# Kernel tuning notes

Hardware: AMD Instinct MI355X
Metric: run time of the kernel (lower is better)

Reference implementation:

```python
import jax, jax.numpy as jnp
import numpy as np

N, C, H, K = 4096, 512, 128, 3
NEG = -jnp.inf


def _linear(x, W, b):
    return x @ W.T + b


def _lrelu(x):
    return jnp.where(x > 0, x, 0.01 * x)  # nn.LeakyReLU default slope


def _cos_sim(x, y):
    # torch cal_cos_similarity: xy / (|x| |y|^T), NaN (0/0) -> 0
    xy = x @ y.T
    den = jnp.linalg.norm(x, axis=1, keepdims=True) * jnp.linalg.norm(y, axis=1, keepdims=True).T
    return xy / jnp.where(den == 0, 1.0, den)


def setup_inputs() -> dict:
    key = jax.random.key(0)
    ks = jax.random.split(key, 24)
    x_hidden = jax.random.normal(ks[0], (N, H), jnp.float32)
    cm = (jax.random.uniform(ks[1], (N, C)) < 0.05).astype(jnp.float32)
    # ensure every concept has at least one member stock (no empty concepts)
    cm = cm.at[jnp.arange(C) % N, jnp.arange(C)].set(1.0)
    market_value = jax.random.uniform(ks[2], (N,), jnp.float32, 0.1, 1.0)
    s = 1.0 / np.sqrt(H)
    inp = {"x_hidden": x_hidden, "concept_matrix": cm, "market_value": market_value}
    names = ["ps", "ps_fore", "ps_back", "hs", "hs_fore", "hs_back", "indi"]
    for i, n in enumerate(names):
        inp[f"W_{n}"] = jax.random.uniform(ks[3 + 2 * i], (H, H), jnp.float32, -s, s)
        inp[f"b_{n}"] = jax.random.uniform(ks[4 + 2 * i], (H,), jnp.float32, -s, s)
    inp["W_out"] = jax.random.uniform(ks[20], (1, H), jnp.float32, -s, s)
    inp["b_out"] = jax.random.uniform(ks[21], (1,), jnp.float32, -s, s)
    return inp


def reference(x_hidden, concept_matrix, market_value,
              W_ps, b_ps, W_ps_fore, b_ps_fore, W_ps_back, b_ps_back,
              W_hs, b_hs, W_hs_fore, b_hs_fore, W_hs_back, b_hs_back,
              W_indi, b_indi, W_out, b_out):
    x = x_hidden
    n = x.shape[0]
    # --- predefined-concept (ps) branch ---
    s2c = concept_matrix * market_value[:, None]                     # [N,C]
    s2c_den = s2c.sum(0)[None, :] * concept_matrix + 1.0
    s2c = s2c / s2c_den
    hidden = s2c.T @ x                                               # [C,H]
    valid1 = hidden.sum(1) != 0                                      # row-filter mask
    s2c2 = jax.nn.softmax(x @ hidden.T, axis=0)                      # softmax over stocks
    hidden = (s2c2.T @ x) * valid1[:, None]                          # [C,H]
    c2s = jax.nn.softmax(jnp.where(valid1[None, :], _cos_sim(x, hidden), NEG), axis=1)
    p_shared = _linear(c2s @ hidden, W_ps, b_ps)
    p_back = _linear(p_shared, W_ps_back, b_ps_back)
    out_ps = _lrelu(_linear(p_shared, W_ps_fore, b_ps_fore))
    # --- hidden-concept (hs) branch ---
    h = x - p_back
    hs2c = _cos_sim(h, h)                                            # [N,N]
    diag = jnp.diagonal(hs2c)
    hs2c = hs2c * (1.0 - jnp.eye(n, dtype=h.dtype))
    idx = jax.lax.top_k(hs2c, K)[1]                                  # [N,K]
    mask = jnp.zeros((n, n), h.dtype).at[jnp.arange(n)[:, None], idx].set(1.0)
    hs2c = hs2c * mask
    hs2c = hs2c + jnp.diag((hs2c.sum(0) != 0).astype(h.dtype) * diag)
    hidden2 = hs2c.T @ h                                             # [N,H]
    valid2 = hidden2.sum(1) != 0
    hidden2 = hidden2 * valid2[:, None]
    hc2s = jax.nn.softmax(jnp.where(valid2[None, :], _cos_sim(h, hidden2), NEG), axis=1)
    h_shared = _linear(hc2s @ hidden2, W_hs, b_hs)
    h_back = _linear(h_shared, W_hs_back, b_hs_back)
    out_hs = _lrelu(_linear(h_shared, W_hs_fore, b_hs_fore))
    # --- individual branch ---
    indiv = x - p_back - h_back
    out_indi = _lrelu(_linear(indiv, W_indi, b_indi))
    all_info = out_ps + out_hs + out_indi
    return _linear(all_info, W_out, b_out).squeeze()                 # [N]
```

## Files before the change

kernel.cpp:

```cpp
#include <hip/hip_runtime.h>
#include <hip/hip_fp16.h>
#include <math.h>

#define N 4096
#define C 512
#define H 128
#define PAD 40

typedef __attribute__((ext_vector_type(8))) short bf16x8;
typedef __attribute__((ext_vector_type(4))) float f32x4;


__device__ inline float wave_reduce_sum(float v) {
#pragma unroll
  for (int m = 32; m; m >>= 1) v += __shfl_xor(v, m);
  return v;
}

__device__ inline float lrelu(float v) { return v > 0.f ? v : 0.01f * v; }

__device__ inline bool better(float v, int j, float w, int k) {
  return (v > w) || (v == w && j < k);
}

__device__ inline void top3_ins(float v, int j, float& v0, int& j0,
                                float& v1, int& j1, float& v2, int& j2) {
  if (better(v, j, v0, j0)) { v2 = v1; j2 = j1; v1 = v0; j1 = j0; v0 = v; j0 = j; }
  else if (better(v, j, v1, j1)) { v2 = v1; j2 = j1; v1 = v; j1 = j; }
  else if (better(v, j, v2, j2)) { v2 = v; j2 = j; }
}

__device__ inline void ins5(float s, int j, float v[5], int jx[5]) {
  if (!better(s, j, v[4], jx[4])) return;
  if (better(s, j, v[0], jx[0])) {
    v[4]=v[3]; jx[4]=jx[3]; v[3]=v[2]; jx[3]=jx[2]; v[2]=v[1]; jx[2]=jx[1];
    v[1]=v[0]; jx[1]=jx[0]; v[0]=s; jx[0]=j;
  } else if (better(s, j, v[1], jx[1])) {
    v[4]=v[3]; jx[4]=jx[3]; v[3]=v[2]; jx[3]=jx[2]; v[2]=v[1]; jx[2]=jx[1];
    v[1]=s; jx[1]=j;
  } else if (better(s, j, v[2], jx[2])) {
    v[4]=v[3]; jx[4]=jx[3]; v[3]=v[2]; jx[3]=jx[2]; v[2]=s; jx[2]=j;
  } else if (better(s, j, v[3], jx[3])) {
    v[4]=v[3]; jx[4]=jx[3]; v[3]=s; jx[3]=j;
  } else {
    v[4]=s; jx[4]=j;
  }
}

__device__ inline unsigned short f2bf(float f) {
  unsigned u = __float_as_uint(f);
  unsigned r = u + 0x7fffu + ((u >> 16) & 1u);
  return (unsigned short)(r >> 16);
}
__device__ inline float bf2f(unsigned short h) {
  return __uint_as_float(((unsigned)h) << 16);
}

__global__ __launch_bounds__(256) void k_split(const float* __restrict__ in,
                                               unsigned short* __restrict__ hi,
                                               unsigned short* __restrict__ lo) {
  int idx = (blockIdx.x * 256 + threadIdx.x) * 4;
  float4 v = *(const float4*)&in[idx];
  float vv[4] = {v.x, v.y, v.z, v.w};
  unsigned short h[4], l[4];
#pragma unroll
  for (int c = 0; c < 4; c++) {
    h[c] = f2bf(vv[c]);
    l[c] = f2bf(vv[c] - bf2f(h[c]));
  }
  uint2 ph = {(unsigned)h[0] | ((unsigned)h[1] << 16),
              (unsigned)h[2] | ((unsigned)h[3] << 16)};
  uint2 pl = {(unsigned)l[0] | ((unsigned)l[1] << 16),
              (unsigned)l[2] | ((unsigned)l[3] << 16)};
  *(uint2*)&hi[idx] = ph;
  *(uint2*)&lo[idx] = pl;
}

__global__ __launch_bounds__(256) void k_tsplit(const float* __restrict__ in,
                                                unsigned short* __restrict__ thi,
                                                unsigned short* __restrict__ tlo,
                                                int R) {
  __shared__ float tile[32][132];
  int r0 = blockIdx.x * 32, tid = threadIdx.x;
#pragma unroll
  for (int q = 0; q < 4; q++) {
    int f = q * 256 + tid;
    int row = f >> 5, ch = f & 31;
    *(float4*)&tile[row][ch * 4] = *(const float4*)&in[(size_t)(r0 + row) * 128 + ch * 4];
  }
  __syncthreads();
  int c = tid & 127, half = tid >> 7;
  unsigned short hh[16], ll[16];
#pragma unroll
  for (int rr = 0; rr < 16; rr++) {
    float v = tile[half * 16 + rr][c];
    hh[rr] = f2bf(v);
    ll[rr] = f2bf(v - bf2f(hh[rr]));
  }
  size_t off = (size_t)c * R + r0 + half * 16;
  uint4 ph0 = {(unsigned)hh[0] | ((unsigned)hh[1] << 16), (unsigned)hh[2] | ((unsigned)hh[3] << 16),
               (unsigned)hh[4] | ((unsigned)hh[5] << 16), (unsigned)hh[6] | ((unsigned)hh[7] << 16)};
  uint4 ph1 = {(unsigned)hh[8] | ((unsigned)hh[9] << 16), (unsigned)hh[10] | ((unsigned)hh[11] << 16),
               (unsigned)hh[12] | ((unsigned)hh[13] << 16), (unsigned)hh[14] | ((unsigned)hh[15] << 16)};
  uint4 pl0 = {(unsigned)ll[0] | ((unsigned)ll[1] << 16), (unsigned)ll[2] | ((unsigned)ll[3] << 16),
               (unsigned)ll[4] | ((unsigned)ll[5] << 16), (unsigned)ll[6] | ((unsigned)ll[7] << 16)};
  uint4 pl1 = {(unsigned)ll[8] | ((unsigned)ll[9] << 16), (unsigned)ll[10] | ((unsigned)ll[11] << 16),
               (unsigned)ll[12] | ((unsigned)ll[13] << 16), (unsigned)ll[14] | ((unsigned)ll[15] << 16)};
  *(uint4*)&thi[off] = ph0; *(uint4*)&thi[off + 8] = ph1;
  *(uint4*)&tlo[off] = pl0; *(uint4*)&tlo[off + 8] = pl1;
}


__global__ __launch_bounds__(64) void k_colsum_s2c(
    const float* __restrict__ cm, const float* __restrict__ mv,
    float* __restrict__ colsum_c) {
  int c = blockIdx.x * 64 + threadIdx.x;
  int i0 = blockIdx.y * 256;
  float acc = 0.f;
  for (int i = i0; i < i0 + 256; i++) acc += cm[(size_t)i * C + c] * mv[i];
  atomicAdd(&colsum_c[c], acc);
}

__global__ __launch_bounds__(64) void k_valid1(const float* __restrict__ hid,
                                               float* __restrict__ valid1) {
  int c = blockIdx.x, t = threadIdx.x;
  float s = hid[(size_t)c * H + t] + hid[(size_t)c * H + 64 + t];
  s = wave_reduce_sum(s);
  if (t == 0) valid1[c] = (s != 0.f) ? 1.f : 0.f;
}

__global__ __launch_bounds__(64) void k_rownorm128(const float* __restrict__ A,
                                                   float* __restrict__ nrm) {
  int r = blockIdx.x, t = threadIdx.x;
  float a = A[(size_t)r * H + t], b = A[(size_t)r * H + 64 + t];
  float ss = wave_reduce_sum(a * a + b * b);
  if (t == 0) nrm[r] = sqrtf(ss);
}

__global__ __launch_bounds__(256) void k_colstats(const float* __restrict__ sc,
                                                  float* __restrict__ colmax,
                                                  float* __restrict__ colsum) {
  __shared__ float red[256];
  int c = blockIdx.x, t = threadIdx.x;
  float v[16];
  float m = -3e38f;
#pragma unroll
  for (int q = 0; q < 16; q++) {
    v[q] = sc[(size_t)(q * 256 + t) * C + c];
    m = fmaxf(m, v[q]);
  }
  red[t] = m; __syncthreads();
  for (int s = 128; s; s >>= 1) { if (t < s) red[t] = fmaxf(red[t], red[t + s]); __syncthreads(); }
  m = red[0]; __syncthreads();
  float sum = 0.f;
#pragma unroll
  for (int q = 0; q < 16; q++) sum += __expf(v[q] - m);
  red[t] = sum; __syncthreads();
  for (int s = 128; s; s >>= 1) { if (t < s) red[t] += red[t + s]; __syncthreads(); }
  if (t == 0) { colmax[c] = m; colsum[c] = red[0]; }
}

__global__ __launch_bounds__(256) void k_cs_softmax(
    const float* __restrict__ sc, const float* __restrict__ xnorm,
    const float* __restrict__ hnorm, const float* __restrict__ valid1,
    unsigned short* __restrict__ cshi, unsigned short* __restrict__ cslo) {
  __shared__ float red[256];
  int i = blockIdx.x, t = threadIdx.x;
  float xn = xnorm[i];
  float r0 = sc[(size_t)i * C + t], r1 = sc[(size_t)i * C + 256 + t];
  float d0 = xn * hnorm[t], d1 = xn * hnorm[256 + t];
  float c0 = r0 / (d0 == 0.f ? 1.f : d0);
  float c1 = r1 / (d1 == 0.f ? 1.f : d1);
  float s0 = (valid1[t] != 0.f) ? c0 : -3e38f;
  float s1 = (valid1[256 + t] != 0.f) ? c1 : -3e38f;
  red[t] = fmaxf(s0, s1); __syncthreads();
  for (int s = 128; s; s >>= 1) { if (t < s) red[t] = fmaxf(red[t], red[t + s]); __syncthreads(); }
  float m = red[0]; __syncthreads();
  float p0 = (s0 > -1e37f) ? __expf(s0 - m) : 0.f;
  float p1 = (s1 > -1e37f) ? __expf(s1 - m) : 0.f;
  red[t] = p0 + p1; __syncthreads();
  for (int s = 128; s; s >>= 1) { if (t < s) red[t] += red[t + s]; __syncthreads(); }
  float inv = 1.f / red[0];
  float a = p0 * inv, b = p1 * inv;
  unsigned short ha = f2bf(a), hb = f2bf(b);
  cshi[(size_t)i * C + t] = ha;
  cslo[(size_t)i * C + t] = f2bf(a - bf2f(ha));
  cshi[(size_t)i * C + 256 + t] = hb;
  cslo[(size_t)i * C + 256 + t] = f2bf(b - bf2f(hb));
}

__global__ __launch_bounds__(64) void k_hhat(const float* __restrict__ h,
                                             float* __restrict__ hhat,
                                             unsigned short* __restrict__ hhi,
                                             unsigned short* __restrict__ hlo,
                                             float* __restrict__ diagv) {
  int i = blockIdx.x, t = threadIdx.x;
  float a = h[(size_t)i * H + t], b = h[(size_t)i * H + 64 + t];
  float ss = wave_reduce_sum(a * a + b * b);
  float hn = sqrtf(ss);
  float den = hn * hn;
  float dg = (den == 0.f) ? 0.f : ss / den;
  float inv = (ss > 0.f) ? (1.f / hn) : 1.f;
  float va = a * inv, vb = b * inv;
  hhat[(size_t)i * H + t] = va;
  hhat[(size_t)i * H + 64 + t] = vb;
  unsigned short ha = f2bf(va), hb = f2bf(vb);
  hhi[(size_t)i * H + t] = ha;
  hlo[(size_t)i * H + t] = f2bf(va - bf2f(ha));
  hhi[(size_t)i * H + 64 + t] = hb;
  hlo[(size_t)i * H + 64 + t] = f2bf(vb - bf2f(hb));
  if (t == 0) diagv[i] = dg;
}

__global__ __launch_bounds__(64) void k_fin_hidden2(
    const float* __restrict__ h, const float* __restrict__ diagv,
    const float* __restrict__ colsum_m, float* __restrict__ hidden2,
    unsigned short* __restrict__ h2hi, unsigned short* __restrict__ h2lo,
    float* __restrict__ valid2f) {
  int j = blockIdx.x, t = threadIdx.x;
  float add = (colsum_m[j] != 0.f) ? diagv[j] : 0.f;
  float a = hidden2[(size_t)j * H + t] + add * h[(size_t)j * H + t];
  float b = hidden2[(size_t)j * H + 64 + t] + add * h[(size_t)j * H + 64 + t];
  float s = a + b, ss = a * a + b * b;
#pragma unroll
  for (int m = 32; m; m >>= 1) { s += __shfl_xor(s, m); ss += __shfl_xor(ss, m); }
  bool valid = (s != 0.f);
  a = valid ? a : 0.f; b = valid ? b : 0.f;
  hidden2[(size_t)j * H + t] = a;
  hidden2[(size_t)j * H + 64 + t] = b;
  float inv = (valid && ss > 0.f) ? (1.f / sqrtf(ss)) : 1.f;
  float va = a * inv, vb = b * inv;
  unsigned short ha = f2bf(va), hb = f2bf(vb);
  h2hi[(size_t)j * H + t] = ha;
  h2lo[(size_t)j * H + t] = f2bf(va - bf2f(ha));
  h2hi[(size_t)j * H + 64 + t] = hb;
  h2lo[(size_t)j * H + 64 + t] = f2bf(vb - bf2f(hb));
  if (t == 0) valid2f[j] = valid ? 1.f : 0.f;
}

__global__ __launch_bounds__(64) void k_final(const float* __restrict__ ai,
                                              const float* __restrict__ Wout,
                                              const float* __restrict__ bout,
                                              float* __restrict__ out) {
  int i = blockIdx.x, t = threadIdx.x;
  float s = ai[(size_t)i * H + t] * Wout[t] + ai[(size_t)i * H + 64 + t] * Wout[64 + t];
  s = wave_reduce_sum(s);
  if (t == 0) out[i] = s + bout[0];
}

template <int EPI>
__global__ __launch_bounds__(256) void k_mfma_nt(
    const unsigned short* __restrict__ Ahi, const unsigned short* __restrict__ Alo,
    const unsigned short* __restrict__ Bhi, const unsigned short* __restrict__ Blo,
    const float* __restrict__ validn, float* __restrict__ out,
    unsigned short* __restrict__ ehi, float* __restrict__ lsum, int Nn) {
  __shared__ __align__(16) unsigned short sAh[128 * PAD];
  __shared__ __align__(16) unsigned short sAl[128 * PAD];
  __shared__ __align__(16) unsigned short sBh[128 * PAD];
  __shared__ __align__(16) unsigned short sBl[128 * PAD];
  int tid = threadIdx.x;
  int bm = blockIdx.y * 128, bn = blockIdx.x * 128;
  int lane = tid & 63, w = tid >> 6;
  int wm = (w & 1) * 64, wn = (w >> 1) * 64;
  int l15 = lane & 15, quad = lane >> 4;
  f32x4 zero = {0.f, 0.f, 0.f, 0.f};
  f32x4 acc[4][4];
#pragma unroll
  for (int mt = 0; mt < 4; mt++)
#pragma unroll
    for (int nt = 0; nt < 4; nt++) acc[mt][nt] = zero;

  for (int kt = 0; kt < 128; kt += 32) {
#pragma unroll
    for (int q = 0; q < 2; q++) {
      int f = tid * 2 + q;
      int row = f >> 2, ch = f & 3;
      size_t ga = (size_t)(bm + row) * 128 + kt + ch * 8;
      size_t gb = (size_t)(bn + row) * 128 + kt + ch * 8;
      int ls = row * PAD + ch * 8;
      *(uint4*)&sAh[ls] = *(const uint4*)&Ahi[ga];
      *(uint4*)&sAl[ls] = *(const uint4*)&Alo[ga];
      *(uint4*)&sBh[ls] = *(const uint4*)&Bhi[gb];
      *(uint4*)&sBl[ls] = *(const uint4*)&Blo[gb];
    }
    __syncthreads();
    bf16x8 ah[4], al[4], bh[4], bl[4];
#pragma unroll
    for (int t = 0; t < 4; t++) {
      int ar = (wm + t * 16 + l15) * PAD + quad * 8;
      ah[t] = *(const bf16x8*)&sAh[ar];
      al[t] = *(const bf16x8*)&sAl[ar];
      int br = (wn + t * 16 + l15) * PAD + quad * 8;
      bh[t] = *(const bf16x8*)&sBh[br];
      bl[t] = *(const bf16x8*)&sBl[br];
    }
#pragma unroll
    for (int mt = 0; mt < 4; mt++)
#pragma unroll
      for (int nt = 0; nt < 4; nt++) {
        acc[mt][nt] = __builtin_amdgcn_mfma_f32_16x16x32_bf16(ah[mt], bh[nt], acc[mt][nt], 0, 0, 0);
        acc[mt][nt] = __builtin_amdgcn_mfma_f32_16x16x32_bf16(ah[mt], bl[nt], acc[mt][nt], 0, 0, 0);
        acc[mt][nt] = __builtin_amdgcn_mfma_f32_16x16x32_bf16(al[mt], bh[nt], acc[mt][nt], 0, 0, 0);
      }
    __syncthreads();
  }
  if (EPI == 3) {
    float vm[4];
#pragma unroll
    for (int nt = 0; nt < 4; nt++) vm[nt] = validn[bn + wn + nt * 16 + l15];
#pragma unroll
    for (int mt = 0; mt < 4; mt++) {
#pragma unroll
      for (int rg = 0; rg < 4; rg++) {
        int row = bm + wm + mt * 16 + quad * 4 + rg;
        float rsum = 0.f;
#pragma unroll
        for (int nt = 0; nt < 4; nt++) {
          int col = bn + wn + nt * 16 + l15;
          float e = (vm[nt] != 0.f) ? __expf(acc[mt][nt][rg] - 1.f) : 0.f;
          rsum += e;
          ehi[(size_t)row * N + col] = f2bf(e);
        }
#pragma unroll
        for (int d = 1; d < 16; d <<= 1) rsum += __shfl_xor(rsum, d);
        if (l15 == 0) atomicAdd(&lsum[row], rsum);
      }
    }
  } else if (EPI == 2) {
#pragma unroll
    for (int mt = 0; mt < 4; mt++) {
// ... 162 lines not shown
  int wm = (w & 1) * 64, wn = (w >> 1) * 64;
  int l15 = lane & 15, quad = lane >> 4;
  f32x4 zero = {0.f, 0.f, 0.f, 0.f};
  f32x4 acc[4][4];
#pragma unroll
  for (int mt = 0; mt < 4; mt++)
#pragma unroll
    for (int nt = 0; nt < 4; nt++) acc[mt][nt] = zero;

  for (int kt = 0; kt < KC; kt += 32) {
    int kr = tid >> 3;
    int mc = (tid & 7) * 16;
    int k = k0 + kt + kr;
    float mvk = (AMODE == 1) ? mv[k] : 0.f;
#pragma unroll
    for (int q = 0; q < 4; q++) {
      int m0 = mc + q * 4;
      float4 pv = *(const float4*)&P[(size_t)k * C + bm + m0];
      float4 c1 = *(const float4*)&col1[bm + m0];
      float wv[4];
      if (AMODE == 1) {
        wv[0] = pv.x * mvk / (c1.x * pv.x + 1.f);
        wv[1] = pv.y * mvk / (c1.y * pv.y + 1.f);
        wv[2] = pv.z * mvk / (c1.z * pv.z + 1.f);
        wv[3] = pv.w * mvk / (c1.w * pv.w + 1.f);
      } else {
        float4 c2 = *(const float4*)&col2[bm + m0];
        wv[0] = __expf(pv.x - c1.x) / c2.x;
        wv[1] = __expf(pv.y - c1.y) / c2.y;
        wv[2] = __expf(pv.z - c1.z) / c2.z;
        wv[3] = __expf(pv.w - c1.w) / c2.w;
      }
#pragma unroll
      for (int j = 0; j < 4; j++) {
        unsigned short hh = f2bf(wv[j]);
        sAh[(m0 + j) * PAD + kr] = hh;
        sAl[(m0 + j) * PAD + kr] = f2bf(wv[j] - bf2f(hh));
      }
    }
#pragma unroll
    for (int q = 0; q < 2; q++) {
      int f = q * 256 + tid;
      int row = f >> 2, ch = f & 3;
      size_t gb = (size_t)row * N + k0 + kt + ch * 8;
      int ls = row * PAD + ch * 8;
      *(uint4*)&sBh[ls] = *(const uint4*)&Bthi[gb];
      *(uint4*)&sBl[ls] = *(const uint4*)&Btlo[gb];
    }
    __syncthreads();
    bf16x8 ah[4], al[4], bh[4], bl[4];
#pragma unroll
    for (int t = 0; t < 4; t++) {
      int ar = (wm + t * 16 + l15) * PAD + quad * 8;
      ah[t] = *(const bf16x8*)&sAh[ar];
      al[t] = *(const bf16x8*)&sAl[ar];
      int br = (wn + t * 16 + l15) * PAD + quad * 8;
      bh[t] = *(const bf16x8*)&sBh[br];
      bl[t] = *(const bf16x8*)&sBl[br];
    }
#pragma unroll
    for (int mt = 0; mt < 4; mt++)
#pragma unroll
      for (int nt = 0; nt < 4; nt++) {
        acc[mt][nt] = __builtin_amdgcn_mfma_f32_16x16x32_bf16(ah[mt], bh[nt], acc[mt][nt], 0, 0, 0);
        acc[mt][nt] = __builtin_amdgcn_mfma_f32_16x16x32_bf16(ah[mt], bl[nt], acc[mt][nt], 0, 0, 0);
        acc[mt][nt] = __builtin_amdgcn_mfma_f32_16x16x32_bf16(al[mt], bh[nt], acc[mt][nt], 0, 0, 0);
      }
    __syncthreads();
  }
  float* pp = partial + (size_t)blockIdx.z * C * 128;
#pragma unroll
  for (int mt = 0; mt < 4; mt++)
#pragma unroll
    for (int nt = 0; nt < 4; nt++) {
      int col = wn + nt * 16 + l15;
#pragma unroll
      for (int rg = 0; rg < 4; rg++) {
        int row = bm + wm + mt * 16 + quad * 4 + rg;
        pp[(size_t)row * 128 + col] = acc[mt][nt][rg];
      }
    }
}

template <int EPI>
__global__ __launch_bounds__(256) void k_mfma_lin(
    const float* __restrict__ A, const float* __restrict__ Wt,
    const float* __restrict__ bias, const float* __restrict__ aux,
    float* __restrict__ out) {
  __shared__ __align__(16) unsigned short sAh[32 * PAD];
  __shared__ __align__(16) unsigned short sAl[32 * PAD];
  __shared__ __align__(16) unsigned short sWh[128 * PAD];
  __shared__ __align__(16) unsigned short sWl[128 * PAD];
  int tid = threadIdx.x;
  int bm = blockIdx.y * 32;
  int lane = tid & 63, w = tid >> 6;
  int rt = (w & 1) * 16, ch2 = (w >> 1) * 64;
  int l15 = lane & 15, quad = lane >> 4;
  f32x4 zero = {0.f, 0.f, 0.f, 0.f};
  f32x4 acc[4];
#pragma unroll
  for (int nt = 0; nt < 4; nt++) acc[nt] = zero;

  for (int kt = 0; kt < 128; kt += 32) {
    {
      int arow = tid >> 3, ach = tid & 7;
      float4 av = *(const float4*)&A[(size_t)(bm + arow) * 128 + kt + ach * 4];
      float aa[4] = {av.x, av.y, av.z, av.w};
      int ls = arow * PAD + ach * 4;
#pragma unroll
      for (int c = 0; c < 4; c++) {
        unsigned short hh = f2bf(aa[c]);
        sAh[ls + c] = hh;
        sAl[ls + c] = f2bf(aa[c] - bf2f(hh));
      }
    }
#pragma unroll
    for (int q = 0; q < 4; q++) {
      int f = q * 256 + tid;
      int wrow = f >> 3, wch = f & 7;
      float4 wv = *(const float4*)&Wt[(size_t)wrow * 128 + kt + wch * 4];
      float ww[4] = {wv.x, wv.y, wv.z, wv.w};
      int ls = wrow * PAD + wch * 4;
#pragma unroll
      for (int c = 0; c < 4; c++) {
        unsigned short hh = f2bf(ww[c]);
        sWh[ls + c] = hh;
        sWl[ls + c] = f2bf(ww[c] - bf2f(hh));
      }
    }
    __syncthreads();
    bf16x8 ah, al, bh[4], bl[4];
    {
      int ar = (rt + l15) * PAD + quad * 8;
      ah = *(const bf16x8*)&sAh[ar];
      al = *(const bf16x8*)&sAl[ar];
    }
#pragma unroll
    for (int nt = 0; nt < 4; nt++) {
      int br = (ch2 + nt * 16 + l15) * PAD + quad * 8;
      bh[nt] = *(const bf16x8*)&sWh[br];
      bl[nt] = *(const bf16x8*)&sWl[br];
    }
#pragma unroll
    for (int nt = 0; nt < 4; nt++) {
      acc[nt] = __builtin_amdgcn_mfma_f32_16x16x32_bf16(ah, bh[nt], acc[nt], 0, 0, 0);
      acc[nt] = __builtin_amdgcn_mfma_f32_16x16x32_bf16(ah, bl[nt], acc[nt], 0, 0, 0);
      acc[nt] = __builtin_amdgcn_mfma_f32_16x16x32_bf16(al, bh[nt], acc[nt], 0, 0, 0);
    }
    __syncthreads();
  }
#pragma unroll
  for (int nt = 0; nt < 4; nt++) {
    int col = ch2 + nt * 16 + l15;
    float bv = bias[col];
#pragma unroll
    for (int rg = 0; rg < 4; rg++) {
      int row = bm + rt + quad * 4 + rg;
      size_t off = (size_t)row * 128 + col;
      float v = acc[nt][rg] + bv;
      if (EPI == 0) out[off] = v;
      else if (EPI == 1) out[off] = lrelu(v);
      else if (EPI == 2) out[off] += lrelu(v);
      else out[off] = aux[off] - v;
    }
  }
}

__global__ __launch_bounds__(256) void k_scatter(
    const float* __restrict__ mtv, const int* __restrict__ mtj,
    const float* __restrict__ h, float* __restrict__ hidden2,
    float* __restrict__ colsum_m) {
  int i = blockIdx.x * 4 + (threadIdx.x >> 6);
  int lane = threadIdx.x & 63;
  float h0 = h[(size_t)i * H + lane], h1 = h[(size_t)i * H + 64 + lane];
#pragma unroll
  for (int s = 0; s < 3; s++) {
    float v = mtv[i * 3 + s];
    int j = mtj[i * 3 + s];
    atomicAdd(&hidden2[(size_t)j * H + lane], v * h0);
    atomicAdd(&hidden2[(size_t)j * H + 64 + lane], v * h1);
    if (lane == s) atomicAdd(&colsum_m[j], v);
  }
}

__global__ __launch_bounds__(256) void k_reduce(
    const float* __restrict__ partial, float* __restrict__ out, int cnt,
    size_t slot, size_t size4, const float* __restrict__ scalem,
    const float* __restrict__ divm, unsigned short* __restrict__ hi,
    unsigned short* __restrict__ lo) {
  size_t idx = (size_t)blockIdx.x * 256 + threadIdx.x;
  if (idx >= size4) return;
  float4 s = {0, 0, 0, 0};
  for (int c = 0; c < cnt; c++) {
    float4 v = *(const float4*)&partial[c * slot + idx * 4];
    s.x += v.x; s.y += v.y; s.z += v.z; s.w += v.w;
  }
  if (scalem) {
    float sc = scalem[idx >> 5];
    s.x *= sc; s.y *= sc; s.z *= sc; s.w *= sc;
  }
  if (divm) {
    float sc = 1.f / divm[idx >> 5];
    s.x *= sc; s.y *= sc; s.z *= sc; s.w *= sc;
  }
  *(float4*)&out[idx * 4] = s;
  if (hi) {
    float vv[4] = {s.x, s.y, s.z, s.w};
    unsigned short h[4], l[4];
#pragma unroll
    for (int c = 0; c < 4; c++) {
      h[c] = f2bf(vv[c]);
      l[c] = f2bf(vv[c] - bf2f(h[c]));
    }
    uint2 ph = {(unsigned)h[0] | ((unsigned)h[1] << 16),
                (unsigned)h[2] | ((unsigned)h[3] << 16)};
    uint2 pl = {(unsigned)l[0] | ((unsigned)l[1] << 16),
                (unsigned)l[2] | ((unsigned)l[3] << 16)};
    *(uint2*)&hi[idx * 4] = ph;
    *(uint2*)&lo[idx * 4] = pl;
  }
}


extern "C" void kernel_launch(void* const* d_in, const int* in_sizes, int n_in,
                              void* d_out, int out_size, void* d_ws, size_t ws_size,
                              hipStream_t stream) {
  (void)in_sizes; (void)n_in; (void)out_size;
  const float* x   = (const float*)d_in[0];
  const float* cm  = (const float*)d_in[1];
  const float* mv  = (const float*)d_in[2];
  const float* W_ps = (const float*)d_in[3],  *b_ps = (const float*)d_in[4];
  const float* W_psf = (const float*)d_in[5], *b_psf = (const float*)d_in[6];
  const float* W_psb = (const float*)d_in[7], *b_psb = (const float*)d_in[8];
  const float* W_hs = (const float*)d_in[9],  *b_hs = (const float*)d_in[10];
  const float* W_hsf = (const float*)d_in[11], *b_hsf = (const float*)d_in[12];
  const float* W_hsb = (const float*)d_in[13], *b_hsb = (const float*)d_in[14];
  const float* W_in = (const float*)d_in[15], *b_in = (const float*)d_in[16];
  const float* W_out = (const float*)d_in[17], *b_out = (const float*)d_in[18];
  float* out = (float*)d_out;

  float* W = (float*)d_ws;
  size_t o = 0;
  auto alloc = [&](size_t n) { float* p = W + o; o += n; return p; };
  float* colsum_c = alloc(C);
  float* colmax   = alloc(C);
  float* colsumexp= alloc(C);
  float* valid1   = alloc(C);
  float* hnorm_ps = alloc(C);
  float* xnorm    = alloc(N);
  float* diagv    = alloc(N);
  float* colsum_m = alloc(N);
  float* valid2f  = alloc(N);
  float* lsum     = alloc(N);
  float* mtv      = alloc(3 * N);
  int*   mtj      = (int*)alloc(3 * N);
  float* hidden1  = alloc((size_t)C * H);
  float* hidden_ps= alloc((size_t)C * H);
  float* scores   = alloc((size_t)N * C);
  float* ps_pre   = alloc((size_t)N * H);
  float* p_shared = alloc((size_t)N * H);
  float* all_info = alloc((size_t)N * H);
  float* hbuf     = alloc((size_t)N * H);
  float* hhat     = alloc((size_t)N * H);
  float* hidden2  = alloc((size_t)N * H);
  unsigned short* xhi    = (unsigned short*)alloc((size_t)N * H / 2);
  unsigned short* xlo    = (unsigned short*)alloc((size_t)N * H / 2);
  unsigned short* hhathi = (unsigned short*)alloc((size_t)N * H / 2);
  unsigned short* hhatlo = (unsigned short*)alloc((size_t)N * H / 2);
  unsigned short* h2hi   = (unsigned short*)alloc((size_t)N * H / 2);
  unsigned short* h2lo   = (unsigned short*)alloc((size_t)N * H / 2);
  unsigned short* h1hi   = (unsigned short*)alloc((size_t)C * H / 2);
  unsigned short* h1lo   = (unsigned short*)alloc((size_t)C * H / 2);
  unsigned short* hpshi  = (unsigned short*)alloc((size_t)C * H / 2);
  unsigned short* hpslo  = (unsigned short*)alloc((size_t)C * H / 2);
  unsigned short* cshi   = (unsigned short*)alloc((size_t)N * C / 2);
  unsigned short* cslo   = (unsigned short*)alloc((size_t)N * C / 2);
  unsigned short* hpst_hi= (unsigned short*)alloc((size_t)H * C / 2);
  unsigned short* hpst_lo= (unsigned short*)alloc((size_t)H * C / 2);
  unsigned short* h2t_hi = (unsigned short*)alloc((size_t)H * N / 2);
  unsigned short* h2t_lo = (unsigned short*)alloc((size_t)H * N / 2);
  unsigned short* xt_hi  = (unsigned short*)alloc((size_t)H * N / 2);
  unsigned short* xt_lo  = (unsigned short*)alloc((size_t)H * N / 2);
  float* Sbuf     = alloc((size_t)N * N / 2);
  unsigned short* Sh  = (unsigned short*)Sbuf;
  unsigned short* Ehi = (unsigned short*)Sbuf;
  float* partial  = W + o;
  size_t rem = ws_size / 4 - o;
  int Z = (rem >= (size_t)16 * N * H) ? 16 : 8;
  int KC = 4096 / Z;

  hipMemsetAsync(colsum_c, 0, C * sizeof(float), stream);
  hipMemsetAsync(colsum_m, 0, N * sizeof(float), stream);
  hipMemsetAsync(lsum, 0, N * sizeof(float), stream);
  hipMemsetAsync(hidden2, 0, (size_t)N * H * sizeof(float), stream);

  dim3 blk(256);
  k_split<<<dim3(N * H / 1024), blk, 0, stream>>>(x, xhi, xlo);
  k_tsplit<<<dim3(N / 32), blk, 0, stream>>>(x, xt_hi, xt_lo, N);
  k_colsum_s2c<<<dim3(C / 64, 16), dim3(64), 0, stream>>>(cm, mv, colsum_c);
  k_mfma_genA<1><<<dim3(1, C / 128, 32), blk, 0, stream>>>(
      cm, mv, colsum_c, nullptr, xt_hi, xt_lo, partial, N / 32);
  k_reduce<<<dim3(C * H / 4 / 256), blk, 0, stream>>>(
      partial, hidden1, 32, (size_t)C * H, (size_t)C * H / 4, nullptr, nullptr,
      h1hi, h1lo);
  k_valid1<<<dim3(C), dim3(64), 0, stream>>>(hidden1, valid1);
  k_mfma_nt<0><<<dim3(C / 128, N / 128), blk, 0, stream>>>(
      xhi, xlo, h1hi, h1lo, nullptr, scores, nullptr, nullptr, C);
  k_colstats<<<dim3(C), blk, 0, stream>>>(scores, colmax, colsumexp);
  k_mfma_genA<2><<<dim3(1, C / 128, 32), blk, 0, stream>>>(
      scores, nullptr, colmax, colsumexp, xt_hi, xt_lo, partial, N / 32);
  k_reduce<<<dim3(C * H / 4 / 256), blk, 0, stream>>>(
      partial, hidden_ps, 32, (size_t)C * H, (size_t)C * H / 4, valid1, nullptr,
      hpshi, hpslo);
  k_rownorm128<<<dim3(N), dim3(64), 0, stream>>>(x, xnorm);
  k_rownorm128<<<dim3(C), dim3(64), 0, stream>>>(hidden_ps, hnorm_ps);
  k_mfma_nt<0><<<dim3(C / 128, N / 128), blk, 0, stream>>>(
      xhi, xlo, hpshi, hpslo, nullptr, scores, nullptr, nullptr, C);
  k_cs_softmax<<<dim3(N), blk, 0, stream>>>(scores, xnorm, hnorm_ps, valid1,
                                            cshi, cslo);
  k_tsplit<<<dim3(C / 32), blk, 0, stream>>>(hidden_ps, hpst_hi, hpst_lo, C);
  k_mfma_kn<1><<<dim3(1, N / 128, 4), blk, 0, stream>>>(
      cshi, cslo, hpst_hi, hpst_lo, partial, C, C / 4);
  k_reduce<<<dim3(N * H / 4 / 256), blk, 0, stream>>>(
      partial, ps_pre, 4, (size_t)N * H, (size_t)N * H / 4, nullptr, nullptr,
      nullptr, nullptr);
  k_mfma_lin<0><<<dim3(1, N / 32), blk, 0, stream>>>(
      ps_pre, W_ps, b_ps, nullptr, p_shared);
  k_mfma_lin<3><<<dim3(1, N / 32), blk, 0, stream>>>(
      p_shared, W_psb, b_psb, x, hbuf);
  k_mfma_lin<1><<<dim3(1, N / 32), blk, 0, stream>>>(
      p_shared, W_psf, b_psf, nullptr, all_info);
  k_hhat<<<dim3(N), dim3(64), 0, stream>>>(hbuf, hhat, hhathi, hhatlo, diagv);
  k_mfma_nt<2><<<dim3(N / 128, N / 128), blk, 0, stream>>>(
      hhathi, hhatlo, hhathi, hhatlo, nullptr, nullptr, Sh, nullptr, N);
  k_rowtop<<<dim3(N / 4), blk, 0, stream>>>(Sh, hhat, mtv, mtj);
  k_scatter<<<dim3(N / 4), blk, 0, stream>>>(mtv, mtj, hbuf, hidden2, colsum_m);
  k_fin_hidden2<<<dim3(N), dim3(64), 0, stream>>>(hbuf, diagv, colsum_m, hidden2,
                                                  h2hi, h2lo, valid2f);
  k_mfma_nt<3><<<dim3(N / 128, N / 128), blk, 0, stream>>>(
      hhathi, hhatlo, h2hi, h2lo, valid2f, nullptr, Ehi, lsum, N);
  k_tsplit<<<dim3(N / 32), blk, 0, stream>>>(hidden2, h2t_hi, h2t_lo, N);
  k_mfma_kn<0><<<dim3(1, N / 128, Z), blk, 0, stream>>>(
      Ehi, nullptr, h2t_hi, h2t_lo, partial, N, KC);
  k_reduce<<<dim3(N * H / 4 / 256), blk, 0, stream>>>(
      partial, ps_pre, Z, (size_t)N * H, (size_t)N * H / 4, nullptr, lsum,
      nullptr, nullptr);
  k_mfma_lin<0><<<dim3(1, N / 32), blk, 0, stream>>>(
      ps_pre, W_hs, b_hs, nullptr, p_shared);
  k_mfma_lin<2><<<dim3(1, N / 32), blk, 0, stream>>>(
      p_shared, W_hsf, b_hsf, nullptr, all_info);
  k_mfma_lin<3><<<dim3(1, N / 32), blk, 0, stream>>>(
      p_shared, W_hsb, b_hsb, hbuf, hbuf);
  k_mfma_lin<2><<<dim3(1, N / 32), blk, 0, stream>>>(
      hbuf, W_in, b_in, nullptr, all_info);
  k_final<<<dim3(N), dim3(64), 0, stream>>>(all_info, W_out, b_out, out);
}
```

Baseline: 419.1 us.

## Fuse linear-layer chains into per-branch tail kernels and fold norms into reductions

Replaces the chains of small k_mfma_lin launches (plus k_hhat and k_final) with two fused kernels, k_ps_tail and k_hs_tail. Each keeps a 32-row tile in LDS and runs its successive 128x128 GEMMs back-to-back, passing intermediates (p_shared, h_shared, indiv) through shared memory instead of global memory. Row norms and the valid masks are now computed inside k_split and k_reduce, which removes the separate k_rownorm128 and k_valid1 launches. The aim is fewer launches and less global traffic, at the cost of heavier blocks that use large LDS (about 103 KB), which limits occupancy and serialises weight loads.

```diff
diff --git a/kernel.cpp b/kernel.cpp
--- a/kernel.cpp
+++ b/kernel.cpp
@@ -6,6 +6,7 @@
 #define C 512
 #define H 128
 #define PAD 40
+#define WP 136
 
 typedef __attribute__((ext_vector_type(8))) short bf16x8;
 typedef __attribute__((ext_vector_type(4))) float f32x4;
@@ -58,13 +59,17 @@
 
 __global__ __launch_bounds__(256) void k_split(const float* __restrict__ in,
                                                unsigned short* __restrict__ hi,
-                                               unsigned short* __restrict__ lo) {
-  int idx = (blockIdx.x * 256 + threadIdx.x) * 4;
+                                               unsigned short* __restrict__ lo,
+                                               float* __restrict__ nrm) {
+  int t = threadIdx.x;
+  int idx = (blockIdx.x * 256 + t) * 4;
   float4 v = *(const float4*)&in[idx];
   float vv[4] = {v.x, v.y, v.z, v.w};
   unsigned short h[4], l[4];
+  float ss = 0.f;
 #pragma unroll
   for (int c = 0; c < 4; c++) {
+    ss += vv[c] * vv[c];
     h[c] = f2bf(vv[c]);
     l[c] = f2bf(vv[c] - bf2f(h[c]));
   }
@@ -74,6 +79,11 @@
               (unsigned)l[2] | ((unsigned)l[3] << 16)};
   *(uint2*)&hi[idx] = ph;
   *(uint2*)&lo[idx] = pl;
+  if (nrm) {
+#pragma unroll
+    for (int m = 16; m; m >>= 1) ss += __shfl_xor(ss, m);
+    if ((t & 31) == 0) nrm[idx >> 7] = sqrtf(ss);
+  }
 }
 
 __global__ __launch_bounds__(256) void k_tsplit(const float* __restrict__ in,
@@ -119,22 +129,6 @@
   float acc = 0.f;
   for (int i = i0; i < i0 + 256; i++) acc += cm[(size_t)i * C + c] * mv[i];
   atomicAdd(&colsum_c[c], acc);
-}
-
-__global__ __launch_bounds__(64) void k_valid1(const float* __restrict__ hid,
-                                               float* __restrict__ valid1) {
-  int c = blockIdx.x, t = threadIdx.x;
-  float s = hid[(size_t)c * H + t] + hid[(size_t)c * H + 64 + t];
-  s = wave_reduce_sum(s);
-  if (t == 0) valid1[c] = (s != 0.f) ? 1.f : 0.f;
-}
-
-__global__ __launch_bounds__(64) void k_rownorm128(const float* __restrict__ A,
-                                                   float* __restrict__ nrm) {
-  int r = blockIdx.x, t = threadIdx.x;
-  float a = A[(size_t)r * H + t], b = A[(size_t)r * H + 64 + t];
-  float ss = wave_reduce_sum(a * a + b * b);
-  if (t == 0) nrm[r] = sqrtf(ss);
 }
 
 __global__ __launch_bounds__(256) void k_colstats(const float* __restrict__ sc,
@@ -189,29 +183,6 @@
   cslo[(size_t)i * C + 256 + t] = f2bf(b - bf2f(hb));
 }
 
-__global__ __launch_bounds__(64) void k_hhat(const float* __restrict__ h,
-                                             float* __restrict__ hhat,
-                                             unsigned short* __restrict__ hhi,
-                                             unsigned short* __restrict__ hlo,
-                                             float* __restrict__ diagv) {
-  int i = blockIdx.x, t = threadIdx.x;
-  float a = h[(size_t)i * H + t], b = h[(size_t)i * H + 64 + t];
-  float ss = wave_reduce_sum(a * a + b * b);
-  float hn = sqrtf(ss);
-  float den = hn * hn;
-  float dg = (den == 0.f) ? 0.f : ss / den;
-  float inv = (ss > 0.f) ? (1.f / hn) : 1.f;
-  float va = a * inv, vb = b * inv;
-  hhat[(size_t)i * H + t] = va;
-  hhat[(size_t)i * H + 64 + t] = vb;
-  unsigned short ha = f2bf(va), hb = f2bf(vb);
-  hhi[(size_t)i * H + t] = ha;
-  hlo[(size_t)i * H + t] = f2bf(va - bf2f(ha));
-  hhi[(size_t)i * H + 64 + t] = hb;
-  hlo[(size_t)i * H + 64 + t] = f2bf(vb - bf2f(hb));
-  if (t == 0) diagv[i] = dg;
-}
-
 __global__ __launch_bounds__(64) void k_fin_hidden2(
     const float* __restrict__ h, const float* __restrict__ diagv,
     const float* __restrict__ colsum_m, float* __restrict__ hidden2,
@@ -236,16 +207,6 @@
   h2hi[(size_t)j * H + 64 + t] = hb;
   h2lo[(size_t)j * H + 64 + t] = f2bf(vb - bf2f(hb));
   if (t == 0) valid2f[j] = valid ? 1.f : 0.f;
-}
-
-__global__ __launch_bounds__(64) void k_final(const float* __restrict__ ai,
-                                              const float* __restrict__ Wout,
-                                              const float* __restrict__ bout,
-                                              float* __restrict__ out) {
-  int i = blockIdx.x, t = threadIdx.x;
-  float s = ai[(size_t)i * H + t] * Wout[t] + ai[(size_t)i * H + 64 + t] * Wout[64 + t];
-  s = wave_reduce_sum(s);
-  if (t == 0) out[i] = s + bout[0];
 }
 
 template <int EPI>
@@ -574,90 +535,6 @@
     }
 }
 
-template <int EPI>
-__global__ __launch_bounds__(256) void k_mfma_lin(
-    const float* __restrict__ A, const float* __restrict__ Wt,
-    const float* __restrict__ bias, const float* __restrict__ aux,
-    float* __restrict__ out) {
-  __shared__ __align__(16) unsigned short sAh[32 * PAD];
-  __shared__ __align__(16) unsigned short sAl[32 * PAD];
-  __shared__ __align__(16) unsigned short sWh[128 * PAD];
-  __shared__ __align__(16) unsigned short sWl[128 * PAD];
-  int tid = threadIdx.x;
-  int bm = blockIdx.y * 32;
-  int lane = tid & 63, w = tid >> 6;
-  int rt = (w & 1) * 16, ch2 = (w >> 1) * 64;
-  int l15 = lane & 15, quad = lane >> 4;
-  f32x4 zero = {0.f, 0.f, 0.f, 0.f};
-  f32x4 acc[4];
-#pragma unroll
-  for (int nt = 0; nt < 4; nt++) acc[nt] = zero;
-
-  for (int kt = 0; kt < 128; kt += 32) {
-    {
-      int arow = tid >> 3, ach = tid & 7;
-      float4 av = *(const float4*)&A[(size_t)(bm + arow) * 128 + kt + ach * 4];
-      float aa[4] = {av.x, av.y, av.z, av.w};
-      int ls = arow * PAD + ach * 4;
-#pragma unroll
-      for (int c = 0; c < 4; c++) {
-        unsigned short hh = f2bf(aa[c]);
-        sAh[ls + c] = hh;
-        sAl[ls + c] = f2bf(aa[c] - bf2f(hh));
-      }
-    }
-#pragma unroll
-    for (int q = 0; q < 4; q++) {
-      int f = q * 256 + tid;
-      int wrow = f >> 3, wch = f & 7;
-      float4 wv = *(const float4*)&Wt[(size_t)wrow * 128 + kt + wch * 4];
-      float ww[4] = {wv.x, wv.y, wv.z, wv.w};
-      int ls = wrow * PAD + wch * 4;
-#pragma unroll
-      for (int c = 0; c < 4; c++) {
-        unsigned short hh = f2bf(ww[c]);
-        sWh[ls + c] = hh;
-        sWl[ls + c] = f2bf(ww[c] - bf2f(hh));
-      }
-    }
-    __syncthreads();
-    bf16x8 ah, al, bh[4], bl[4];
-    {
-      int ar = (rt + l15) * PAD + quad * 8;
-      ah = *(const bf16x8*)&sAh[ar];
-      al = *(const bf16x8*)&sAl[ar];
-    }
-#pragma unroll
-    for (int nt = 0; nt < 4; nt++) {
-      int br = (ch2 + nt * 16 + l15) * PAD + quad * 8;
-      bh[nt] = *(const bf16x8*)&sWh[br];
-      bl[nt] = *(const bf16x8*)&sWl[br];
-    }
-#pragma unroll
-    for (int nt = 0; nt < 4; nt++) {
-      acc[nt] = __builtin_amdgcn_mfma_f32_16x16x32_bf16(ah, bh[nt], acc[nt], 0, 0, 0);
-      acc[nt] = __builtin_amdgcn_mfma_f32_16x16x32_bf16(ah, bl[nt], acc[nt], 0, 0, 0);
-      acc[nt] = __builtin_amdgcn_mfma_f32_16x16x32_bf16(al, bh[nt], acc[nt], 0, 0, 0);
-    }
-    __syncthreads();
-  }
-#pragma unroll
-  for (int nt = 0; nt < 4; nt++) {
-    int col = ch2 + nt * 16 + l15;
-    float bv = bias[col];
-#pragma unroll
-    for (int rg = 0; rg < 4; rg++) {
-      int row = bm + rt + quad * 4 + rg;
-      size_t off = (size_t)row * 128 + col;
-      float v = acc[nt][rg] + bv;
-      if (EPI == 0) out[off] = v;
-      else if (EPI == 1) out[off] = lrelu(v);
-      else if (EPI == 2) out[off] += lrelu(v);
-      else out[off] = aux[off] - v;
-    }
-  }
-}
-
 __global__ __launch_bounds__(256) void k_scatter(
     const float* __restrict__ mtv, const int* __restrict__ mtj,
     const float* __restrict__ h, float* __restrict__ hidden2,
@@ -679,7 +556,8 @@
     const float* __restrict__ partial, float* __restrict__ out, int cnt,
     size_t slot, size_t size4, const float* __restrict__ scalem,
     const float* __restrict__ divm, unsigned short* __restrict__ hi,
-    unsigned short* __restrict__ lo) {
+    unsigned short* __restrict__ lo, float* __restrict__ nrmout,
+    float* __restrict__ validout) {
   size_t idx = (size_t)blockIdx.x * 256 + threadIdx.x;
   if (idx >= size4) return;
   float4 s = {0, 0, 0, 0};
@@ -710,6 +588,303 @@
                 (unsigned)l[2] | ((unsigned)l[3] << 16)};
     *(uint2*)&hi[idx * 4] = ph;
     *(uint2*)&lo[idx * 4] = pl;
+  }
+  if (nrmout || validout) {
+    float rs = s.x + s.y + s.z + s.w;
+    float rq = s.x * s.x + s.y * s.y + s.z * s.z + s.w * s.w;
+#pragma unroll
+    for (int m = 16; m; m >>= 1) { rs += __shfl_xor(rs, m); rq += __shfl_xor(rq, m); }
+    if ((threadIdx.x & 31) == 0) {
+      if (nrmout) nrmout[idx >> 5] = sqrtf(rq);
+      if (validout) validout[idx >> 5] = (rs != 0.f) ? 1.f : 0.f;
+    }
+  }
+}
+
+
+#define LOAD_W(Wt)                                                        \
+  do {                                                                    \
+    _Pragma("unroll") for (int q = 0; q < 16; q++) {                      \
+      int f = q * 256 + tid;                                              \
+      int wr = f >> 5, wc = (f & 31) * 4;                                 \
+      float4 wv = *(const float4*)&(Wt)[(size_t)wr * 128 + wc];           \
+      float ww[4] = {wv.x, wv.y, wv.z, wv.w};                             \
+      _Pragma("unroll") for (int c = 0; c < 4; c++) {                     \
+        unsigned short hh = f2bf(ww[c]);                                  \
+        sWh[wr * WP + wc + c] = hh;                                       \
+        sWl[wr * WP + wc + c] = f2bf(ww[c] - bf2f(hh));                   \
+      }                                                                   \
+    }                                                                     \
+  } while (0)
+
+#define GEMM32(accv)                                                              \
+  do {                                                                            \
+    _Pragma("unroll") for (int nt = 0; nt < 4; nt++) accv[nt] = zero;             \
+    _Pragma("unroll") for (int kt = 0; kt < 128; kt += 32) {                      \
+      bf16x8 ah = *(const bf16x8*)&sAh[(rt + l15) * WP + kt + quad * 8];          \
+      bf16x8 al = *(const bf16x8*)&sAl[(rt + l15) * WP + kt + quad * 8];          \
+      _Pragma("unroll") for (int nt = 0; nt < 4; nt++) {                          \
+        int br = (ch2 + nt * 16 + l15) * WP + kt + quad * 8;                      \
+        bf16x8 bh = *(const bf16x8*)&sWh[br];                                     \
+        bf16x8 bl = *(const bf16x8*)&sWl[br];                                     \
+        accv[nt] = __builtin_amdgcn_mfma_f32_16x16x32_bf16(ah, bh, accv[nt], 0, 0, 0); \
+        accv[nt] = __builtin_amdgcn_mfma_f32_16x16x32_bf16(ah, bl, accv[nt], 0, 0, 0); \
+        accv[nt] = __builtin_amdgcn_mfma_f32_16x16x32_bf16(al, bh, accv[nt], 0, 0, 0); \
+      }                                                                           \
+    }                                                                             \
+  } while (0)
+
+__global__ __launch_bounds__(256) void k_ps_tail(
+    const float* __restrict__ A, const float* __restrict__ x,
+    const float* __restrict__ W_ps, const float* __restrict__ b_ps,
+    const float* __restrict__ W_psb, const float* __restrict__ b_psb,
+    const float* __restrict__ W_psf, const float* __restrict__ b_psf,
+    float* __restrict__ hbuf, float* __restrict__ hhat,
+    unsigned short* __restrict__ hhi, unsigned short* __restrict__ hlo,
+    float* __restrict__ diagv, float* __restrict__ all_info) {
+  __shared__ __align__(16) unsigned short sWh[128 * WP];
+  __shared__ __align__(16) unsigned short sWl[128 * WP];
+  __shared__ __align__(16) unsigned short sAh[32 * WP];
+  __shared__ __align__(16) unsigned short sAl[32 * WP];
+  __shared__ __align__(16) float sF[32][132];
+  int tid = threadIdx.x;
+  int bm = blockIdx.x * 32;
+  int lane = tid & 63, w = tid >> 6;
+  int rt = (w & 1) * 16, ch2 = (w >> 1) * 64;
+  int l15 = lane & 15, quad = lane >> 4;
+  f32x4 zero = {0.f, 0.f, 0.f, 0.f};
+  f32x4 acc[4];
+
+  {
+    int row = tid >> 3, c0 = (tid & 7) * 16;
+    const float* src = &A[(size_t)(bm + row) * 128 + c0];
+#pragma unroll
+    for (int q = 0; q < 4; q++) {
+      float4 v = *(const float4*)&src[q * 4];
+      float vv[4] = {v.x, v.y, v.z, v.w};
+#pragma unroll
+      for (int c = 0; c < 4; c++) {
+        unsigned short hh = f2bf(vv[c]);
+        sAh[row * WP + c0 + q * 4 + c] = hh;
+        sAl[row * WP + c0 + q * 4 + c] = f2bf(vv[c] - bf2f(hh));
+      }
+    }
+  }
+  LOAD_W(W_ps);
+  __syncthreads();
+  GEMM32(acc);
+  __syncthreads();
+#pragma unroll
+  for (int nt = 0; nt < 4; nt++) {
+    int col = ch2 + nt * 16 + l15;
+    float bv = b_ps[col];
+#pragma unroll
+    for (int rg = 0; rg < 4; rg++) {
+      int row = rt + quad * 4 + rg;
+      float v = acc[nt][rg] + bv;
+      unsigned short hh = f2bf(v);
+      sAh[row * WP + col] = hh;
+      sAl[row * WP + col] = f2bf(v - bf2f(hh));
+    }
+  }
+  LOAD_W(W_psb);
+  __syncthreads();
+  GEMM32(acc);
+#pragma unroll
+  for (int nt = 0; nt < 4; nt++) {
+    int col = ch2 + nt * 16 + l15;
+    float bv = b_psb[col];
+#pragma unroll
+    for (int rg = 0; rg < 4; rg++) {
+      int row = rt + quad * 4 + rg;
+      size_t off = (size_t)(bm + row) * 128 + col;
+      float hv = x[off] - (acc[nt][rg] + bv);
+      hbuf[off] = hv;
+      sF[row][col] = hv;
+    }
+  }
+  __syncthreads();
+  {
+    int row = tid >> 3, c0 = (tid & 7) * 16;
+    float hv16[16];
+    float ssp = 0.f;
+#pragma unroll
+    for (int q = 0; q < 16; q++) {
+      float v = sF[row][c0 + q];
+      hv16[q] = v;
+      ssp += v * v;
+    }
+    ssp += __shfl_xor(ssp, 1);
+    ssp += __shfl_xor(ssp, 2);
+    ssp += __shfl_xor(ssp, 4);
+    float ss = ssp;
+    float hn = sqrtf(ss);
+    float den = hn * hn;
+    float dg = (den == 0.f) ? 0.f : ss / den;
+    float inv = (ss > 0.f) ? (1.f / hn) : 1.f;
+    size_t base = (size_t)(bm + row) * H + c0;
+    float va16[16];
+    unsigned short hh16[16], ll16[16];
+#pragma unroll
+    for (int q = 0; q < 16; q++) {
+      va16[q] = hv16[q] * inv;
+      hh16[q] = f2bf(va16[q]);
+      ll16[q] = f2bf(va16[q] - bf2f(hh16[q]));
+    }
+#pragma unroll
+    for (int q4 = 0; q4 < 4; q4++) {
+      float4 fv = {va16[q4 * 4], va16[q4 * 4 + 1], va16[q4 * 4 + 2], va16[q4 * 4 + 3]};
+      *(float4*)&hhat[base + q4 * 4] = fv;
+    }
+    uint4 ph0 = {(unsigned)hh16[0] | ((unsigned)hh16[1] << 16), (unsigned)hh16[2] | ((unsigned)hh16[3] << 16),
+                 (unsigned)hh16[4] | ((unsigned)hh16[5] << 16), (unsigned)hh16[6] | ((unsigned)hh16[7] << 16)};
+    uint4 ph1 = {(unsigned)hh16[8] | ((unsigned)hh16[9] << 16), (unsigned)hh16[10] | ((unsigned)hh16[11] << 16),
+                 (unsigned)hh16[12] | ((unsigned)hh16[13] << 16), (unsigned)hh16[14] | ((unsigned)hh16[15] << 16)};
+    uint4 pl0 = {(unsigned)ll16[0] | ((unsigned)ll16[1] << 16), (unsigned)ll16[2] | ((unsigned)ll16[3] << 16),
+                 (unsigned)ll16[4] | ((unsigned)ll16[5] << 16), (unsigned)ll16[6] | ((unsigned)ll16[7] << 16)};
+    uint4 pl1 = {(unsigned)ll16[8] | ((unsigned)ll16[9] << 16), (unsigned)ll16[10] | ((unsigned)ll16[11] << 16),
+                 (unsigned)ll16[12] | ((unsigned)ll16[13] << 16), (unsigned)ll16[14] | ((unsigned)ll16[15] << 16)};
+    *(uint4*)&hhi[base] = ph0; *(uint4*)&hhi[base + 8] = ph1;
+    *(uint4*)&hlo[base] = pl0; *(uint4*)&hlo[base + 8] = pl1;
+    if ((tid & 7) == 0) diagv[bm + row] = dg;
+  }
+  LOAD_W(W_psf);
+  __syncthreads();
+  GEMM32(acc);
+#pragma unroll
+  for (int nt = 0; nt < 4; nt++) {
+    int col = ch2 + nt * 16 + l15;
+    float bv = b_psf[col];
+#pragma unroll
+    for (int rg = 0; rg < 4; rg++) {
+      int row = rt + quad * 4 + rg;
+      size_t off = (size_t)(bm + row) * 128 + col;
+      all_info[off] = lrelu(acc[nt][rg] + bv);
+    }
+  }
+}
+
+__global__ __launch_bounds__(256) void k_hs_tail(
+    const float* __restrict__ A, const float* __restrict__ hbuf,
+    const float* __restrict__ all_info,
+    const float* __restrict__ W_hs, const float* __restrict__ b_hs,
+    const float* __restrict__ W_hsf, const float* __restrict__ b_hsf,
+    const float* __restrict__ W_hsb, const float* __restrict__ b_hsb,
+    const float* __restrict__ W_in, const float* __restrict__ b_in,
+    const float* __restrict__ W_out, const float* __restrict__ b_out,
+    float* __restrict__ out) {
+  __shared__ __align__(16) unsigned short sWh[128 * WP];
+  __shared__ __align__(16) unsigned short sWl[128 * WP];
+  __shared__ __align__(16) unsigned short sAh[32 * WP];
+  __shared__ __align__(16) unsigned short sAl[32 * WP];
+  __shared__ __align__(16) float sF[32][132];
+  int tid = threadIdx.x;
+  int bm = blockIdx.x * 32;
+  int lane = tid & 63, w = tid >> 6;
+  int rt = (w & 1) * 16, ch2 = (w >> 1) * 64;
+  int l15 = lane & 15, quad = lane >> 4;
+  f32x4 zero = {0.f, 0.f, 0.f, 0.f};
+  f32x4 acc[4];
+  float allv[4][4];
+
+  {
+    int row = tid >> 3, c0 = (tid & 7) * 16;
+    const float* src = &A[(size_t)(bm + row) * 128 + c0];
+#pragma unroll
+    for (int q = 0; q < 4; q++) {
+      float4 v = *(const float4*)&src[q * 4];
+      float vv[4] = {v.x, v.y, v.z, v.w};
+#pragma unroll
+      for (int c = 0; c < 4; c++) {
+        unsigned short hh = f2bf(vv[c]);
+        sAh[row * WP + c0 + q * 4 + c] = hh;
+        sAl[row * WP + c0 + q * 4 + c] = f2bf(vv[c] - bf2f(hh));
+      }
+    }
+  }
+  LOAD_W(W_hs);
+  __syncthreads();
+  GEMM32(acc);
+  __syncthreads();
+#pragma unroll
+  for (int nt = 0; nt < 4; nt++) {
+    int col = ch2 + nt * 16 + l15;
+    float bv = b_hs[col];
+#pragma unroll
+    for (int rg = 0; rg < 4; rg++) {
+      int row = rt + quad * 4 + rg;
+      float v = acc[nt][rg] + bv;
+      unsigned short hh = f2bf(v);
+      sAh[row * WP + col] = hh;
+      sAl[row * WP + col] = f2bf(v - bf2f(hh));
+    }
+  }
+  LOAD_W(W_hsf);
+  __syncthreads();
+  GEMM32(acc);
+#pragma unroll
+  for (int nt = 0; nt < 4; nt++) {
+    int col = ch2 + nt * 16 + l15;
+    float bv = b_hsf[col];
+#pragma unroll
+    for (int rg = 0; rg < 4; rg++) {
+      int row = rt + quad * 4 + rg;
+      size_t off = (size_t)(bm + row) * 128 + col;
+      allv[nt][rg] = all_info[off] + lrelu(acc[nt][rg] + bv);
+    }
+  }
+  __syncthreads();
+  LOAD_W(W_hsb);
+  __syncthreads();
+  GEMM32(acc);
+  float iv[4][4];
+#pragma unroll
+  for (int nt = 0; nt < 4; nt++) {
+    int col = ch2 + nt * 16 + l15;
+    float bv = b_hsb[col];
+#pragma unroll
+    for (int rg = 0; rg < 4; rg++) {
+      int row = rt + quad * 4 + rg;
+      size_t off = (size_t)(bm + row) * 128 + col;
+      iv[nt][rg] = hbuf[off] - (acc[nt][rg] + bv);
+    }
+  }
+  __syncthreads();
+#pragma unroll
+  for (int nt = 0; nt < 4; nt++) {
+    int col = ch2 + nt * 16 + l15;
+#pragma unroll
+    for (int rg = 0; rg < 4; rg++) {
+      int row = rt + quad * 4 + rg;
+      unsigned short hh = f2bf(iv[nt][rg]);
+      sAh[row * WP + col] = hh;
+      sAl[row * WP + col] = f2bf(iv[nt][rg] - bf2f(hh));
+    }
+  }
+  LOAD_W(W_in);
+  __syncthreads();
+  GEMM32(acc);
+#pragma unroll
+  for (int nt = 0; nt < 4; nt++) {
+    int col = ch2 + nt * 16 + l15;
+    float bv = b_in[col];
+#pragma unroll
+    for (int rg = 0; rg < 4; rg++) {
+      int row = rt + quad * 4 + rg;
+      allv[nt][rg] += lrelu(acc[nt][rg] + bv);
+      sF[row][col] = allv[nt][rg];
+    }
+  }
+  __syncthreads();
+  {
+    int row = tid >> 3, c0 = (tid & 7) * 16;
+    float s = 0.f;
+#pragma unroll
+    for (int q = 0; q < 16; q++) s += sF[row][c0 + q] * W_out[c0 + q];
+    s += __shfl_xor(s, 1);
+    s += __shfl_xor(s, 2);
+    s += __shfl_xor(s, 4);
+    if ((tid & 7) == 0) out[bm + row] = s + b_out[0];
   }
 }
 
@@ -750,7 +925,6 @@
   float* hidden_ps= alloc((size_t)C * H);
   float* scores   = alloc((size_t)N * C);
   float* ps_pre   = alloc((size_t)N * H);
-  float* p_shared = alloc((size_t)N * H);
   float* all_info = alloc((size_t)N * H);
   float* hbuf     = alloc((size_t)N * H);
   float* hhat     = alloc((size_t)N * H);
@@ -787,15 +961,14 @@
   hipMemsetAsync(hidden2, 0, (size_t)N * H * sizeof(float), stream);
 
   dim3 blk(256);
-  k_split<<<dim3(N * H / 1024), blk, 0, stream>>>(x, xhi, xlo);
+  k_split<<<dim3(N * H / 1024), blk, 0, stream>>>(x, xhi, xlo, xnorm);
   k_tsplit<<<dim3(N / 32), blk, 0, stream>>>(x, xt_hi, xt_lo, N);
   k_colsum_s2c<<<dim3(C / 64, 16), dim3(64), 0, stream>>>(cm, mv, colsum_c);
   k_mfma_genA<1><<<dim3(1, C / 128, 32), blk, 0, stream>>>(
       cm, mv, colsum_c, nullptr, xt_hi, xt_lo, partial, N / 32);
   k_reduce<<<dim3(C * H / 4 / 256), blk, 0, stream>>>(
       partial, hidden1, 32, (size_t)C * H, (size_t)C * H / 4, nullptr, nullptr,
-      h1hi, h1lo);
-  k_valid1<<<dim3(C), dim3(64), 0, stream>>>(hidden1, valid1);
+      h1hi, h1lo, nullptr, valid1);
   k_mfma_nt<0><<<dim3(C / 128, N / 128), blk, 0, stream>>>(
       xhi, xlo, h1hi, h1lo, nullptr, scores, nullptr, nullptr, C);
   k_colstats<<<dim3(C), blk, 0, stream>>>(scores, colmax, colsumexp);
@@ -803,9 +976,7 @@
       scores, nullptr, colmax, colsumexp, xt_hi, xt_lo, partial, N / 32);
   k_reduce<<<dim3(C * H / 4 / 256), blk, 0, stream>>>(
       partial, hidden_ps, 32, (size_t)C * H, (size_t)C * H / 4, valid1, nullptr,
-      hpshi, hpslo);
-  k_rownorm128<<<dim3(N), dim3(64), 0, stream>>>(x, xnorm);
-  k_rownorm128<<<dim3(C), dim3(64), 0, stream>>>(hidden_ps, hnorm_ps);
+      hpshi, hpslo, hnorm_ps, nullptr);
   k_mfma_nt<0><<<dim3(C / 128, N / 128), blk, 0, stream>>>(
       xhi, xlo, hpshi, hpslo, nullptr, scores, nullptr, nullptr, C);
   k_cs_softmax<<<dim3(N), blk, 0, stream>>>(scores, xnorm, hnorm_ps, valid1,
@@ -815,14 +986,10 @@
       cshi, cslo, hpst_hi, hpst_lo, partial, C, C / 4);
   k_reduce<<<dim3(N * H / 4 / 256), blk, 0, stream>>>(
       partial, ps_pre, 4, (size_t)N * H, (size_t)N * H / 4, nullptr, nullptr,
-      nullptr, nullptr);
-  k_mfma_lin<0><<<dim3(1, N / 32), blk, 0, stream>>>(
-      ps_pre, W_ps, b_ps, nullptr, p_shared);
-  k_mfma_lin<3><<<dim3(1, N / 32), blk, 0, stream>>>(
-      p_shared, W_psb, b_psb, x, hbuf);
-  k_mfma_lin<1><<<dim3(1, N / 32), blk, 0, stream>>>(
-      p_shared, W_psf, b_psf, nullptr, all_info);
-  k_hhat<<<dim3(N), dim3(64), 0, stream>>>(hbuf, hhat, hhathi, hhatlo, diagv);
+      nullptr, nullptr, nullptr, nullptr);
+  k_ps_tail<<<dim3(N / 32), blk, 0, stream>>>(
+      ps_pre, x, W_ps, b_ps, W_psb, b_psb, W_psf, b_psf,
+      hbuf, hhat, hhathi, hhatlo, diagv, all_info);
   k_mfma_nt<2><<<dim3(N / 128, N / 128), blk, 0, stream>>>(
       hhathi, hhatlo, hhathi, hhatlo, nullptr, nullptr, Sh, nullptr, N);
   k_rowtop<<<dim3(N / 4), blk, 0, stream>>>(Sh, hhat, mtv, mtj);
@@ -836,14 +1003,8 @@
       Ehi, nullptr, h2t_hi, h2t_lo, partial, N, KC);
   k_reduce<<<dim3(N * H / 4 / 256), blk, 0, stream>>>(
       partial, ps_pre, Z, (size_t)N * H, (size_t)N * H / 4, nullptr, lsum,
-      nullptr, nullptr);
-  k_mfma_lin<0><<<dim3(1, N / 32), blk, 0, stream>>>(
-      ps_pre, W_hs, b_hs, nullptr, p_shared);
-  k_mfma_lin<2><<<dim3(1, N / 32), blk, 0, stream>>>(
-      p_shared, W_hsf, b_hsf, nullptr, all_info);
-  k_mfma_lin<3><<<dim3(1, N / 32), blk, 0, stream>>>(
-      p_shared, W_hsb, b_hsb, hbuf, hbuf);
-  k_mfma_lin<2><<<dim3(1, N / 32), blk, 0, stream>>>(
-      hbuf, W_in, b_in, nullptr, all_info);
-  k_final<<<dim3(N), dim3(64), 0, stream>>>(all_info, W_out, b_out, out);
-}
+      nullptr, nullptr, nullptr, nullptr);
+  k_hs_tail<<<dim3(N / 32), blk, 0, stream>>>(
+      ps_pre, hbuf, all_info, W_hs, b_hs, W_hsf, b_hsf, W_hsb, b_hsb,
+      W_in, b_in, W_out, b_out, out);
+}
```

After: 388.1 us. 7.4% less time.
